# Kernel optimization log

Measured on AMD Instinct MI355X. Metric: run time of the kernel, lower is better.

Reference implementation:

```python
import jax, jax.numpy as jnp
import numpy as np

TOP_K = 3


def setup_inputs() -> dict:
    key = jax.random.key(0)
    k1, k2, k3 = jax.random.split(key, 3)
    bs, nw, ns, nq = 2, 5, 5, 5
    f_dim, f_h, f_w = 64, 21, 21
    n_img = bs * nw * (ns + nq)
    fm = jax.random.normal(k1, (n_img, f_dim, f_h, f_w), dtype=jnp.float32)
    elabel = jax.random.randint(k2, (n_img,), 0, nw)
    glabel = jax.random.randint(k3, (n_img,), 0, nw)
    return {"fm": fm, "elabel": elabel, "glabel": glabel,
            "bs": bs, "nw": nw, "ns": ns, "nq": nq}


def reference(fm, elabel, glabel, bs, nw, ns, nq):
    _, f_dim, f_h, f_w = fm.shape
    # L2-normalize each spatial descriptor along the channel axis
    fm = fm / (jnp.linalg.norm(fm, axis=1, keepdims=True) + 1e-12)
    fm6 = fm.reshape(bs, nw, ns + nq, f_dim, f_h, f_w)
    sup_fm = fm6[:, :, :ns]   # [bs, nw, ns, c, h, w]
    que_fm = fm6[:, :, ns:]   # [bs, nw, nq, c, h, w]
    # queries: [bs, nw*nq, f_h*f_w, f_dim]
    que = que_fm.reshape(bs, nw * nq, f_dim, f_h * f_w).transpose(0, 1, 3, 2)
    # supports: [bs, nw, ns*f_h*f_w, f_dim]
    sup = sup_fm.transpose(0, 1, 2, 4, 5, 3).reshape(bs, nw, ns * f_h * f_w, f_dim)
    # cosine similarity of every query descriptor to every support descriptor
    # sim: [bs, nw*nq, nw, f_h*f_w, ns*f_h*f_w]
    sim = jnp.einsum('bqxc,bwyc->bqwxy', que, sup)
    # per-query-descriptor top-k nearest support descriptors, summed
    vals, _ = jax.lax.top_k(sim, TOP_K)          # [bs, q, nw, x, k]
    pred = vals.sum(axis=(-2, -1))               # [bs, nw*nq, nw]
    el = elabel.reshape(bs, nw, ns + nq)[:, :, ns:].reshape(-1)
    return pred, el
```

## Files before the change

### kernel.cpp

```cpp
#include <hip/hip_runtime.h>
#include <hip/hip_bf16.h>
#include <math.h>
#include <limits.h>

#define BS 2
#define NW 5
#define NS 5
#define NQ 5
#define FDIM 64
#define FH 21
#define FW 21
#define NPOS (FH*FW)
#define NIMG (BS*NW*(NS+NQ))
#define NQIMG 50
#define IMG_ELEMS (FDIM*NPOS)
#define NY (NS*NPOS)
#define QROWS 448
#define SROWS 2304
#define NSLICE 12
#define NT_S 12
#define NBLK 250
#define NBLK_SIM (NBLK*NSLICE)
#define TILE_B 1024

typedef __attribute__((ext_vector_type(4))) int int4v;

static __device__ __forceinline__ unsigned short f2bf(float x) {
    union { float f; unsigned u; } v; v.f = x;
    unsigned r = v.u + 0x7fffu + ((v.u >> 16) & 1u);
    return (unsigned short)(r >> 16);
}

static __device__ __forceinline__ float bf2f(unsigned short u) {
    union { unsigned u; float f; } v; v.u = ((unsigned)u) << 16;
    return v.f;
}

static __device__ __forceinline__ void gload_lds16(const void* g, void* l) {
    __builtin_amdgcn_global_load_lds((const __attribute__((address_space(1))) void*)g,
                                     (__attribute__((address_space(3))) void*)l, 16, 0, 0);
}

static __device__ __forceinline__ int med3i(int a, int b, int c) {
    int r;
    asm("v_med3_i32 %0, %1, %2, %3" : "=v"(r) : "v"(a), "v"(b), "v"(c));
    return r;
}

#define T3R(d, a0, a1, a2) do { \
    int _n0 = ((d) > (a0)) ? (d) : (a0); \
    int _n1 = med3i((d), (a0), (a1)); \
    int _n2 = med3i((d), (a1), (a2)); \
    (a0) = _n0; (a1) = _n1; (a2) = _n2; } while (0)

#define T3R4(p, i) do { \
    T3R((p)[0], t0[i], t1[i], t2[i]); \
    T3R((p)[1], t0[i], t1[i], t2[i]); \
    T3R((p)[2], t0[i], t1[i], t2[i]); \
    T3R((p)[3], t0[i], t1[i], t2[i]); } while (0)

#define T3F(d, a0, a1, a2) do { \
    float _n0 = fmaxf((d), (a0)); \
    float _n1 = __builtin_amdgcn_fmed3f((d), (a0), (a1)); \
    float _n2 = __builtin_amdgcn_fmed3f((d), (a1), (a2)); \
    (a0) = _n0; (a1) = _n1; (a2) = _n2; } while (0)

__global__ __launch_bounds__(256) void dn4_normalize(const float* __restrict__ fm,
                                                     const int* __restrict__ elabel,
                                                     char* __restrict__ Qn,
                                                     char* __restrict__ Sn,
                                                     float* __restrict__ out) {
    int gid = blockIdx.x * blockDim.x + threadIdx.x;
    if (gid < 50) {
        int bb = gid / 25, rem = gid % 25, wq = rem / 5, qi = rem % 5;
        out[250 + gid] = (float)elabel[(bb * NW + wq) * (NS + NQ) + NS + qi];
    }
    if (gid < 3960) {
        int mat = gid / 396, rem = gid % 396, rr = rem >> 2, k = rem & 3;
        int4v zv = {0, 0, 0, 0};
        *(int4v*)(Sn + (size_t)mat * (SROWS * FDIM) + (size_t)(NY + rr) * FDIM + k * 16) = zv;
    }
    if (gid >= NIMG * NPOS) return;
    int img = gid / NPOS;
    int pos = gid - img * NPOS;
    const float* src = fm + (size_t)img * IMG_ELEMS + pos;
    float v[FDIM];
    float ss = 0.f;
#pragma unroll
    for (int c = 0; c < FDIM; ++c) {
        float x = src[(size_t)c * NPOS];
        v[c] = x;
        ss += x * x;
    }
    float rn = 127.0f / (sqrtf(ss) + 1e-12f);
    int w[16];
#pragma unroll
    for (int k = 0; k < 16; ++k) {
        int q0 = __float2int_rn(v[4 * k]     * rn);
        int q1 = __float2int_rn(v[4 * k + 1] * rn);
        int q2 = __float2int_rn(v[4 * k + 2] * rn);
        int q3 = __float2int_rn(v[4 * k + 3] * rn);
        w[k] = (q0 & 0xff) | ((q1 & 0xff) << 8) | ((q2 & 0xff) << 16) | (q3 << 24);
    }
    char* dst;
    int i10 = img % 10;
    if (i10 < NS) {
        int bw = img / 10;
        dst = Sn + (size_t)bw * (SROWS * FDIM) + (size_t)(i10 * NPOS + pos) * FDIM;
    } else {
        int qidx = (img / 10) * NQ + (i10 - NS);
        dst = Qn + (size_t)qidx * (QROWS * FDIM) + (size_t)pos * FDIM;
    }
#pragma unroll
    for (int k = 0; k < 4; ++k) {
        int4v t = {w[4 * k], w[4 * k + 1], w[4 * k + 2], w[4 * k + 3]};
        *(int4v*)(dst + 16 * k) = t;
    }
}

__global__ __launch_bounds__(256, 6) void dn4_sim_mfma(const char* __restrict__ Qn,
                                                       const char* __restrict__ Sn,
                                                       unsigned short* __restrict__ gtop3) {
    __shared__ __align__(16) char stile[NT_S][TILE_B];

    int orig = blockIdx.x;
    int unit = (orig & 7) * (NBLK_SIM / 8) + (orig >> 3);
    int bid = unit / NSLICE, ys = unit % NSLICE;

    int w = bid % NW;
    int q = (bid / NW) % (NW * NQ);
    int b = bid / (NW * NW * NQ);
    int wq = q / NQ, qi = q % NQ;
    int qidx = (b * NW + wq) * NQ + qi;

    const char* qbase = Qn + (size_t)qidx * (QROWS * FDIM);
    const char* sbase = Sn + (size_t)(b * NW + w) * (SROWS * FDIM);

    int t = threadIdx.x;
    int lane = t & 63, wv = t >> 6;
    int lo16 = lane & 15, hi4 = lane >> 4;

    int stg0 = ((lane >> 2) * FDIM) + ((((lane & 3) ^ ((lane >> 3) & 3)) << 4));
    int tbase = ys * NT_S;

    for (int i = wv; i < NT_S; i += 4)
        gload_lds16(sbase + (size_t)(tbase + i) * TILE_B + stg0, &stile[i][0]);

    int4v bq[7];
#pragma unroll
    for (int i = 0; i < 7; ++i) {
        int xt = wv * 7 + i;
        bq[i] = *(const int4v*)(qbase + (size_t)(xt * 16 + lo16) * FDIM + hi4 * 16);
    }

    asm volatile("s_waitcnt vmcnt(0)" ::: "memory");
    __syncthreads();

    int t0[7], t1[7], t2[7];
#pragma unroll
    for (int i = 0; i < 7; ++i) { t0[i] = INT_MIN; t1[i] = INT_MIN; t2[i] = INT_MIN; }

    int4v zc = {0, 0, 0, 0};

    int rd = lo16 * FDIM + ((hi4 ^ ((lo16 >> 1) & 3)) << 4);

    int4v ca = *(const int4v*)(&stile[0][0] + rd);
    for (int tt = 0; tt < NT_S; ++tt) {
        int4v na = ca;
        if (tt + 1 < NT_S) na = *(const int4v*)(&stile[tt + 1][0] + rd);
        int4v pA = __builtin_amdgcn_mfma_i32_16x16x64_i8(ca, bq[0], zc, 0, 0, 0);
        int4v pB = __builtin_amdgcn_mfma_i32_16x16x64_i8(ca, bq[1], zc, 0, 0, 0);
        T3R4(pA, 0);
        int4v pC = __builtin_amdgcn_mfma_i32_16x16x64_i8(ca, bq[2], zc, 0, 0, 0);
        T3R4(pB, 1);
        int4v pD = __builtin_amdgcn_mfma_i32_16x16x64_i8(ca, bq[3], zc, 0, 0, 0);
        T3R4(pC, 2);
        int4v pE = __builtin_amdgcn_mfma_i32_16x16x64_i8(ca, bq[4], zc, 0, 0, 0);
        T3R4(pD, 3);
        int4v pF = __builtin_amdgcn_mfma_i32_16x16x64_i8(ca, bq[5], zc, 0, 0, 0);
        T3R4(pE, 4);
        int4v pG = __builtin_amdgcn_mfma_i32_16x16x64_i8(ca, bq[6], zc, 0, 0, 0);
        T3R4(pF, 5);
        T3R4(pG, 6);
        ca = na;
    }

    const float INV = 1.0f / 16129.0f;
#pragma unroll
    for (int i = 0; i < 7; ++i) {
        int a0 = t0[i], a1 = t1[i], a2 = t2[i];
#pragma unroll
        for (int mk = 16; mk <= 32; mk <<= 1) {
            int c0 = __shfl_xor(a0, mk, 64);
            int c1 = __shfl_xor(a1, mk, 64);
            int c2 = __shfl_xor(a2, mk, 64);
            T3R(c0, a0, a1, a2);
            T3R(c1, a0, a1, a2);
            T3R(c2, a0, a1, a2);
        }
        if (hi4 == 0) {
            int x = (wv * 7 + i) * 16 + lo16;
            unsigned short* dst = gtop3 + ((size_t)(bid * QROWS + x) * NSLICE + ys) * 3;
            dst[0] = f2bf((float)a0 * INV);
            dst[1] = f2bf((float)a1 * INV);
            dst[2] = f2bf((float)a2 * INV);
        }
    }
}

__global__ __launch_bounds__(448) void dn4_merge(const unsigned short* __restrict__ gtop3,
                                                 float* __restrict__ out) {
    __shared__ float red[7];
    int bid = blockIdx.x;
    int t = threadIdx.x, lane = t & 63, wv = t >> 6;
    const unsigned* p = (const unsigned*)(gtop3 + (size_t)(bid * QROWS + t) * (NSLICE * 3));
    float v[36];
#pragma unroll
    for (int j = 0; j < 18; ++j) {
        unsigned u = p[j];
        v[2 * j]     = bf2f((unsigned short)(u & 0xffffu));
        v[2 * j + 1] = bf2f((unsigned short)(u >> 16));
    }
    float a0 = v[0], a1 = v[1], a2 = v[2];
#pragma unroll
    for (int j = 3; j < 36; ++j) T3F(v[j], a0, a1, a2);
    float s = (t < NPOS) ? (a0 + a1 + a2) : 0.f;
#pragma unroll
    for (int off = 32; off >= 1; off >>= 1) s += __shfl_xor(s, off, 64);
    if (lane == 0) red[wv] = s;
    __syncthreads();
    if (t == 0) {
        float tot = 0.f;
#pragma unroll
        for (int i = 0; i < 7; ++i) tot += red[i];
        out[bid] = tot;
    }
}

extern "C" void kernel_launch(void* const* d_in, const int* in_sizes, int n_in,
                              void* d_out, int out_size, void* d_ws, size_t ws_size,
                              hipStream_t stream) {
    const float* fm     = (const float*)d_in[0];
    const int*   elabel = (const int*)d_in[1];
    float* out = (float*)d_out;

    char* Qn = (char*)d_ws;
    char* Sn = Qn + (size_t)NQIMG * QROWS * FDIM;
    unsigned short* gtop3 = (unsigned short*)(Sn + (size_t)10 * SROWS * FDIM);

    int nthreads = NIMG * NPOS;
    dn4_normalize<<<(nthreads + 255) / 256, 256, 0, stream>>>(fm, elabel, Qn, Sn, out);
    dn4_sim_mfma<<<NBLK_SIM, 256, 0, stream>>>(Qn, Sn, gtop3);
    dn4_merge<<<NBLK, 448, 0, stream>>>(gtop3, out);
}
```

Measured before the change: 50.35 us.

## Switch similarity kernel to 32x32x32 int8 MFMA with larger support slices

Replaces the 16x16x64 int8 MFMA tiling with 32x32x32 MFMA, so each wave handles two 32-row query groups and the top-3 update runs over 16 accumulator values per instruction pair. The support dimension is padded to 2208 rows and split into 3 slices of 23 tiles instead of 12 slices of 12 tiles, with 448-thread blocks and a new XCD-aware block remap. This cuts the number of blocks and the partial top-3 entries the merge kernel must reduce, at the cost of larger LDS use per block and possibly lower occupancy and less parallelism.

Measured after the change: 44.06 us (median of 2 runs). 1.14x faster.

```diff
diff --git a/kernel.cpp b/kernel.cpp
--- a/kernel.cpp
+++ b/kernel.cpp
@@ -16,14 +16,15 @@
 #define IMG_ELEMS (FDIM*NPOS)
 #define NY (NS*NPOS)
 #define QROWS 448
-#define SROWS 2304
-#define NSLICE 12
-#define NT_S 12
+#define SROWS 2208
+#define NSLICE 3
+#define NT_S 23
 #define NBLK 250
 #define NBLK_SIM (NBLK*NSLICE)
-#define TILE_B 1024
-
-typedef __attribute__((ext_vector_type(4))) int int4v;
+#define TILE_B 2048
+
+typedef __attribute__((ext_vector_type(4)))  int int4v;
+typedef __attribute__((ext_vector_type(16))) int int16v;
 
 static __device__ __forceinline__ unsigned short f2bf(float x) {
     union { float f; unsigned u; } v; v.f = x;
@@ -52,12 +53,6 @@
     int _n1 = med3i((d), (a0), (a1)); \
     int _n2 = med3i((d), (a1), (a2)); \
     (a0) = _n0; (a1) = _n1; (a2) = _n2; } while (0)
-
-#define T3R4(p, i) do { \
-    T3R((p)[0], t0[i], t1[i], t2[i]); \
-    T3R((p)[1], t0[i], t1[i], t2[i]); \
-    T3R((p)[2], t0[i], t1[i], t2[i]); \
-    T3R((p)[3], t0[i], t1[i], t2[i]); } while (0)
 
 #define T3F(d, a0, a1, a2) do { \
     float _n0 = fmaxf((d), (a0)); \
@@ -75,8 +70,8 @@
         int bb = gid / 25, rem = gid % 25, wq = rem / 5, qi = rem % 5;
         out[250 + gid] = (float)elabel[(bb * NW + wq) * (NS + NQ) + NS + qi];
     }
-    if (gid < 3960) {
-        int mat = gid / 396, rem = gid % 396, rr = rem >> 2, k = rem & 3;
+    if (gid < 120) {
+        int mat = gid / 12, rr = (gid % 12) >> 2, k = gid & 3;
         int4v zv = {0, 0, 0, 0};
         *(int4v*)(Sn + (size_t)mat * (SROWS * FDIM) + (size_t)(NY + rr) * FDIM + k * 16) = zv;
     }
@@ -118,13 +113,14 @@
     }
 }
 
-__global__ __launch_bounds__(256, 6) void dn4_sim_mfma(const char* __restrict__ Qn,
+__global__ __launch_bounds__(448, 5) void dn4_sim_mfma(const char* __restrict__ Qn,
                                                        const char* __restrict__ Sn,
                                                        unsigned short* __restrict__ gtop3) {
     __shared__ __align__(16) char stile[NT_S][TILE_B];
 
     int orig = blockIdx.x;
-    int unit = (orig & 7) * (NBLK_SIM / 8) + (orig >> 3);
+    int xcd = orig & 7, idx = orig >> 3;
+    int unit = (xcd < 6 ? xcd * 94 : 6 * 94 + (xcd - 6) * 93) + idx;
     int bid = unit / NSLICE, ys = unit % NSLICE;
 
     int w = bid % NW;
@@ -138,72 +134,74 @@
 
     int t = threadIdx.x;
     int lane = t & 63, wv = t >> 6;
-    int lo16 = lane & 15, hi4 = lane >> 4;
+    int l5 = lane & 31, h = lane >> 5;
 
     int stg0 = ((lane >> 2) * FDIM) + ((((lane & 3) ^ ((lane >> 3) & 3)) << 4));
     int tbase = ys * NT_S;
 
-    for (int i = wv; i < NT_S; i += 4)
-        gload_lds16(sbase + (size_t)(tbase + i) * TILE_B + stg0, &stile[i][0]);
-
-    int4v bq[7];
-#pragma unroll
-    for (int i = 0; i < 7; ++i) {
-        int xt = wv * 7 + i;
-        bq[i] = *(const int4v*)(qbase + (size_t)(xt * 16 + lo16) * FDIM + hi4 * 16);
+    for (int i = wv; i < 2 * NT_S; i += 7) {
+        int tile = i >> 1, hh = i & 1;
+        gload_lds16(sbase + (size_t)(tbase + tile) * TILE_B + hh * 1024 + stg0,
+                    &stile[tile][hh * 1024]);
+    }
+
+    int4v bq[2][2];
+#pragma unroll
+    for (int j = 0; j < 2; ++j) {
+        int x = (wv * 2 + j) * 32 + l5;
+        const char* qp = qbase + (size_t)x * FDIM + h * 16;
+        bq[j][0] = *(const int4v*)(qp);
+        bq[j][1] = *(const int4v*)(qp + 32);
     }
 
     asm volatile("s_waitcnt vmcnt(0)" ::: "memory");
     __syncthreads();
 
-    int t0[7], t1[7], t2[7];
-#pragma unroll
-    for (int i = 0; i < 7; ++i) { t0[i] = INT_MIN; t1[i] = INT_MIN; t2[i] = INT_MIN; }
-
-    int4v zc = {0, 0, 0, 0};
-
-    int rd = lo16 * FDIM + ((hi4 ^ ((lo16 >> 1) & 3)) << 4);
-
-    int4v ca = *(const int4v*)(&stile[0][0] + rd);
+    int t0[2], t1[2], t2[2];
+#pragma unroll
+    for (int j = 0; j < 2; ++j) { t0[j] = INT_MIN; t1[j] = INT_MIN; t2[j] = INT_MIN; }
+
+    int16v zc = {0,0,0,0, 0,0,0,0, 0,0,0,0, 0,0,0,0};
+
+    int rd0 = l5 * FDIM + (((0 + h) ^ ((l5 >> 1) & 3)) << 4);
+    int rd1 = l5 * FDIM + (((2 + h) ^ ((l5 >> 1) & 3)) << 4);
+
+    int4v a0 = *(const int4v*)(&stile[0][0] + rd0);
+    int4v a1 = *(const int4v*)(&stile[0][0] + rd1);
     for (int tt = 0; tt < NT_S; ++tt) {
-        int4v na = ca;
-        if (tt + 1 < NT_S) na = *(const int4v*)(&stile[tt + 1][0] + rd);
-        int4v pA = __builtin_amdgcn_mfma_i32_16x16x64_i8(ca, bq[0], zc, 0, 0, 0);
-        int4v pB = __builtin_amdgcn_mfma_i32_16x16x64_i8(ca, bq[1], zc, 0, 0, 0);
-        T3R4(pA, 0);
-        int4v pC = __builtin_amdgcn_mfma_i32_16x16x64_i8(ca, bq[2], zc, 0, 0, 0);
-        T3R4(pB, 1);
-        int4v pD = __builtin_amdgcn_mfma_i32_16x16x64_i8(ca, bq[3], zc, 0, 0, 0);
-        T3R4(pC, 2);
-        int4v pE = __builtin_amdgcn_mfma_i32_16x16x64_i8(ca, bq[4], zc, 0, 0, 0);
-        T3R4(pD, 3);
-        int4v pF = __builtin_amdgcn_mfma_i32_16x16x64_i8(ca, bq[5], zc, 0, 0, 0);
-        T3R4(pE, 4);
-        int4v pG = __builtin_amdgcn_mfma_i32_16x16x64_i8(ca, bq[6], zc, 0, 0, 0);
-        T3R4(pF, 5);
-        T3R4(pG, 6);
-        ca = na;
+        int4v na0 = a0, na1 = a1;
+        if (tt + 1 < NT_S) {
+            na0 = *(const int4v*)(&stile[tt + 1][0] + rd0);
+            na1 = *(const int4v*)(&stile[tt + 1][0] + rd1);
+        }
+        int16v dA = __builtin_amdgcn_mfma_i32_32x32x32_i8(a0, bq[0][0], zc, 0, 0, 0);
+        dA = __builtin_amdgcn_mfma_i32_32x32x32_i8(a1, bq[0][1], dA, 0, 0, 0);
+        int16v dB = __builtin_amdgcn_mfma_i32_32x32x32_i8(a0, bq[1][0], zc, 0, 0, 0);
+        dB = __builtin_amdgcn_mfma_i32_32x32x32_i8(a1, bq[1][1], dB, 0, 0, 0);
+#pragma unroll
+        for (int r = 0; r < 16; ++r) {
+            T3R(dA[r], t0[0], t1[0], t2[0]);
+            T3R(dB[r], t0[1], t1[1], t2[1]);
+        }
+        a0 = na0; a1 = na1;
     }
 
     const float INV = 1.0f / 16129.0f;
 #pragma unroll
-    for (int i = 0; i < 7; ++i) {
-        int a0 = t0[i], a1 = t1[i], a2 = t2[i];
-#pragma unroll
-        for (int mk = 16; mk <= 32; mk <<= 1) {
-            int c0 = __shfl_xor(a0, mk, 64);
-            int c1 = __shfl_xor(a1, mk, 64);
-            int c2 = __shfl_xor(a2, mk, 64);
-            T3R(c0, a0, a1, a2);
-            T3R(c1, a0, a1, a2);
-            T3R(c2, a0, a1, a2);
-        }
-        if (hi4 == 0) {
-            int x = (wv * 7 + i) * 16 + lo16;
+    for (int j = 0; j < 2; ++j) {
+        int a0_ = t0[j], a1_ = t1[j], a2_ = t2[j];
+        int c0 = __shfl_xor(a0_, 32, 64);
+        int c1 = __shfl_xor(a1_, 32, 64);
+        int c2 = __shfl_xor(a2_, 32, 64);
+        T3R(c0, a0_, a1_, a2_);
+        T3R(c1, a0_, a1_, a2_);
+        T3R(c2, a0_, a1_, a2_);
+        if (h == 0) {
+            int x = (wv * 2 + j) * 32 + l5;
             unsigned short* dst = gtop3 + ((size_t)(bid * QROWS + x) * NSLICE + ys) * 3;
-            dst[0] = f2bf((float)a0 * INV);
-            dst[1] = f2bf((float)a1 * INV);
-            dst[2] = f2bf((float)a2 * INV);
+            dst[0] = f2bf((float)a0_ * INV);
+            dst[1] = f2bf((float)a1_ * INV);
+            dst[2] = f2bf((float)a2_ * INV);
         }
     }
 }
@@ -213,17 +211,13 @@
     __shared__ float red[7];
     int bid = blockIdx.x;
     int t = threadIdx.x, lane = t & 63, wv = t >> 6;
-    const unsigned* p = (const unsigned*)(gtop3 + (size_t)(bid * QROWS + t) * (NSLICE * 3));
-    float v[36];
-#pragma unroll
-    for (int j = 0; j < 18; ++j) {
-        unsigned u = p[j];
-        v[2 * j]     = bf2f((unsigned short)(u & 0xffffu));
-        v[2 * j + 1] = bf2f((unsigned short)(u >> 16));
-    }
+    const unsigned short* p = gtop3 + (size_t)(bid * QROWS + t) * (NSLICE * 3);
+    float v[9];
+#pragma unroll
+    for (int j = 0; j < 9; ++j) v[j] = bf2f(p[j]);
     float a0 = v[0], a1 = v[1], a2 = v[2];
 #pragma unroll
-    for (int j = 3; j < 36; ++j) T3F(v[j], a0, a1, a2);
+    for (int j = 3; j < 9; ++j) T3F(v[j], a0, a1, a2);
     float s = (t < NPOS) ? (a0 + a1 + a2) : 0.f;
 #pragma unroll
     for (int off = 32; off >= 1; off >>= 1) s += __shfl_xor(s, off, 64);
@@ -250,6 +244,6 @@
 
     int nthreads = NIMG * NPOS;
     dn4_normalize<<<(nthreads + 255) / 256, 256, 0, stream>>>(fm, elabel, Qn, Sn, out);
-    dn4_sim_mfma<<<NBLK_SIM, 256, 0, stream>>>(Qn, Sn, gtop3);
+    dn4_sim_mfma<<<NBLK_SIM, 448, 0, stream>>>(Qn, Sn, gtop3);
     dn4_merge<<<NBLK, 448, 0, stream>>>(gtop3, out);
 }
```
